# Kernel tuning notes

Hardware: AMD Instinct MI355X
Metric: run time of the kernel (lower is better)

The kernel has to match this reference:

```python
import jax, jax.numpy as jnp
from jax import lax
import numpy as np

B, R, NOBJ, SIZE = 16, 64, 32, 64  # batch, rels/image, objs/image, map size


def setup_inputs() -> dict:
    key = jax.random.key(0)
    ks = jax.random.split(key, 8)
    # boxes as (x1, y1, x2, y2) in an arbitrary image coordinate frame
    xy1 = jax.random.uniform(ks[0], (B, NOBJ, 2), dtype=jnp.float32) * 80.0
    wh = jax.random.uniform(ks[1], (B, NOBJ, 2), dtype=jnp.float32) * 40.0 + 2.0
    bboxes = jnp.concatenate([xy1, xy1 + wh], axis=-1)  # [B, NOBJ, 4]
    num_obj = jnp.full((B,), NOBJ, dtype=jnp.int32)
    num_relation = jnp.full((B,), R, dtype=jnp.int32)  # constant -> static tot_num_rels
    object_pairs = jax.random.randint(ks[2], (B, R, 2), 0, NOBJ)
    conv1_w = jax.random.normal(ks[3], (64, 2, 5, 5), dtype=jnp.float32) * 0.1
    conv1_b = jnp.zeros((64,), dtype=jnp.float32)
    conv2_w = jax.random.normal(ks[4], (32, 64, 5, 5), dtype=jnp.float32) * 0.05
    conv2_b = jnp.zeros((32,), dtype=jnp.float32)
    fc_w = jax.random.normal(ks[5], (512, 32), dtype=jnp.float32) * 0.1
    fc_b = jnp.zeros((512,), dtype=jnp.float32)
    return dict(bboxes=bboxes, num_obj=num_obj, num_relation=num_relation,
                object_pairs=object_pairs, conv1_w=conv1_w, conv1_b=conv1_b,
                conv2_w=conv2_w, conv2_b=conv2_b, fc_w=fc_w, fc_b=fc_b)


def _sp_maps(bboxes, object_pairs):
    # Vectorized replacement of the per-relation python loop + get_sp:
    # both boxes of a pair are rescaled into the 64x64 frame of their union
    # box and rasterized as binary masks (iCAN-style 2-channel spatial config).
    Bc, Rc, _ = object_pairs.shape
    pairs = object_pairs.reshape(-1, 2)                      # [T, 2]
    b_idx = jnp.repeat(jnp.arange(Bc), Rc)                   # [T]
    b0 = bboxes[b_idx, pairs[:, 0]]                          # [T, 4]
    b1 = bboxes[b_idx, pairs[:, 1]]                          # [T, 4]
    ux1 = jnp.minimum(b0[:, 0], b1[:, 0])
    uy1 = jnp.minimum(b0[:, 1], b1[:, 1])
    ux2 = jnp.maximum(b0[:, 2], b1[:, 2])
    uy2 = jnp.maximum(b0[:, 3], b1[:, 3])
    uw = jnp.maximum(ux2 - ux1, 1e-6)
    uh = jnp.maximum(uy2 - uy1, 1e-6)

    def scale(b):  # union-normalized box in [0, SIZE] grid coords
        return jnp.stack([(b[:, 0] - ux1) / uw * SIZE,
                          (b[:, 1] - uy1) / uh * SIZE,
                          (b[:, 2] - ux1) / uw * SIZE,
                          (b[:, 3] - uy1) / uh * SIZE], axis=-1)

    coords = jnp.arange(SIZE, dtype=jnp.float32) + 0.5
    gx = coords[None, None, :]   # [1, 1, SIZE]
    gy = coords[None, :, None]   # [1, SIZE, 1]

    def rasterize(sb):  # sb: [T, 4] -> [T, SIZE, SIZE]
        x1 = sb[:, 0, None, None]; y1 = sb[:, 1, None, None]
        x2 = sb[:, 2, None, None]; y2 = sb[:, 3, None, None]
        return ((gx >= x1) & (gx <= x2) & (gy >= y1) & (gy <= y2)).astype(jnp.float32)

    return jnp.stack([rasterize(scale(b0)), rasterize(scale(b1))], axis=1)  # [T,2,64,64]


def _conv(x, w, b):
    y = lax.conv_general_dilated(x, w, window_strides=(1, 1), padding='VALID',
                                 dimension_numbers=('NCHW', 'OIHW', 'NCHW'))
    return y + b[None, :, None, None]


def _maxpool2(x):
    return lax.reduce_window(x, -jnp.inf, lax.max, (1, 1, 2, 2), (1, 1, 2, 2), 'VALID')


def reference(bboxes, num_obj, num_relation, object_pairs,
              conv1_w, conv1_b, conv2_w, conv2_b, fc_w, fc_b):
    sp = _sp_maps(bboxes, object_pairs)        # [T, 2, 64, 64]
    x = _maxpool2(_conv(sp, conv1_w, conv1_b)) # [T, 64, 30, 30]
    x = _maxpool2(_conv(x, conv2_w, conv2_b))  # [T, 32, 13, 13]
    x = jnp.mean(x, axis=(2, 3))               # AvgPool((13,13)) -> [T, 32]
    return jax.nn.relu(x @ fc_w.T + fc_b)      # [T, 512]
```

## Files before the change

### kernel.cpp

```cpp
#include <hip/hip_runtime.h>
#include <stdint.h>

typedef unsigned long long u64;
typedef short v8s __attribute__((ext_vector_type(8)));
typedef float v4f __attribute__((ext_vector_type(4)));

__device__ __forceinline__ unsigned short f2bf_rne(float f) {
  union { float f; unsigned u; } c; c.f = f;
  unsigned u = c.u;
  u += 0x7fffu + ((u >> 16) & 1u);
  return (unsigned short)(u >> 16);
}

__device__ __forceinline__ void bacc(uint4 z, uint4 a, float* S) {
  const unsigned* zp = &z.x;
  const unsigned* ap = &a.x;
  #pragma unroll
  for (int k = 0; k < 4; k++) {
    unsigned zu = zp[k], au = ap[k];
    S[2 * k]     += __uint_as_float(zu << 16)         - __uint_as_float(au << 16);
    S[2 * k + 1] += __uint_as_float(zu & 0xffff0000u) - __uint_as_float(au & 0xffff0000u);
  }
}


__global__ __launch_bounds__(512) void prepack_g(
    const float* __restrict__ w1,
    unsigned short* __restrict__ Gt)
{
  int e = blockIdx.x * 512 + threadIdx.x;
  int ch = e / 6144, r = e - ch * 6144;
  int cls = r / 384, r2 = r - cls * 384;
  int j = r2 / 64, cout = r2 - j * 64;
  float v = 0.f;
  if (cls > 0) {
    int ia = 0, ib = 0;
    #pragma unroll
    for (int bb = 0; bb < 5; bb++) {
      int base = (bb * (bb + 1)) / 2 + 1;
      if (cls >= base && cls <= base + bb) { ib = bb; ia = cls - base; }
    }
    for (int i = ia; i <= ib; i++)
      for (int jj = 0; jj < j; jj++)
        v += w1[(cout * 2 + ch) * 25 + i * 5 + jj];
  }
  Gt[e] = f2bf_rne(v);
}

__global__ __launch_bounds__(512, 8) void conv1_kernel(
    const float* __restrict__ bboxes,
    const int*   __restrict__ pairs,
    const unsigned short* __restrict__ Gt,
    const float* __restrict__ b1,
    const float* __restrict__ w2,
    unsigned short* __restrict__ XsG,
    unsigned short* __restrict__ Wr)
{
  const int t = threadIdx.x;
  if (blockIdx.x >= 1024) {
    int bb2 = blockIdx.x - 1024;
    #pragma unroll
    for (int r = 0; r < 4; r++) {
      int idx = bb2 * 2048 + r * 512 + t;
      int c = idx / 1600, rem = idx - c * 1600;
      int h = rem / 800, r2 = rem - h * 800;
      int tap = r2 >> 5, chh = r2 & 31;
      Wr[h * 25600 + c * 800 + r2] =
          f2bf_rne(w2[(c * 64 + h * 32 + chh) * 25 + tap]);
    }
    return;
  }
  extern __shared__ char smem[];

  const int n = blockIdx.x;
  const int lane = t & 63;

  {
    const uint4* src = (const uint4*)Gt;
    uint4* dst = (uint4*)smem;
    #pragma unroll
    for (int i = 0; i < 3; i++) dst[t + i * 512] = src[t + i * 512];
  }

  const int bb = n >> 6, rr_ = n & 63;
  const int p0 = pairs[(bb * 64 + rr_) * 2 + 0];
  const int p1 = pairs[(bb * 64 + rr_) * 2 + 1];
  const float* A  = bboxes + (bb * 32 + p0) * 4;
  const float* Bq = bboxes + (bb * 32 + p1) * 4;
  const float ax1 = A[0],  ay1 = A[1],  ax2 = A[2],  ay2 = A[3];
  const float cx1 = Bq[0], cy1 = Bq[1], cx2 = Bq[2], cy2 = Bq[3];
  const float ux1 = fminf(ax1, cx1), uy1 = fminf(ay1, cy1);
  const float ux2 = fmaxf(ax2, cx2), uy2 = fmaxf(ay2, cy2);
  const float uw = fmaxf(ux2 - ux1, 1e-6f), uh = fmaxf(uy2 - uy1, 1e-6f);
  const float g = (float)lane + 0.5f;
  u64 ixs[2], iys[2];
  {
    float X1 = (ax1 - ux1) / uw * 64.f, X2 = (ax2 - ux1) / uw * 64.f;
    float Y1 = (ay1 - uy1) / uh * 64.f, Y2 = (ay2 - uy1) / uh * 64.f;
    ixs[0] = __ballot(g >= X1 && g <= X2);
    iys[0] = __ballot(g >= Y1 && g <= Y2);
  }
  {
    float X1 = (cx1 - ux1) / uw * 64.f, X2 = (cx2 - ux1) / uw * 64.f;
    float Y1 = (cy1 - uy1) / uh * 64.f, Y2 = (cy2 - uy1) / uh * 64.f;
    ixs[1] = __ballot(g >= X1 && g <= X2);
    iys[1] = __ballot(g >= Y1 && g <= Y2);
  }
  __syncthreads();

  const int cg = t & 7, cgo = cg * 16, pr = t >> 3;
  const int hW = cg >> 2;
  float b1v[8];
  #pragma unroll
  for (int i = 0; i < 8; i++) b1v[i] = b1[cg * 8 + i];
  char* const Xbase = (char*)XsG + (u64)n * 115200 + hW * 57600;
  for (int pass = 0; pass < 15; pass++) {
    int pix = pr + (pass << 6);
    if (pix < 900) {
      int qy = pix / 30, qx = pix - qy * 30;
      int cb[2][2], ja_[2][2], jb_[2][2];
      #pragma unroll
      for (int ch = 0; ch < 2; ch++) {
        #pragma unroll
        for (int dy = 0; dy < 2; dy++) {
          unsigned m = (unsigned)(iys[ch] >> (2 * qy + dy)) & 31u;
          int ia = __ffs((int)m) - 1; if (ia < 0) ia = 0;
          int ib = 31 - __clz((int)(m | 1u));
          int cls = m ? (((ib * (ib + 1)) >> 1) + ia + 1) : 0;
          cb[ch][dy] = (ch * 16 + cls) * 768 + cgo;
        }
        #pragma unroll
        for (int dx = 0; dx < 2; dx++) {
          unsigned mx = (unsigned)(ixs[ch] >> (2 * qx + dx)) & 31u;
          int ja = __ffs((int)mx) - 1; if (ja < 0) ja = 0;
          int jbp = mx ? (32 - __clz((int)mx)) : 0;
          ja_[ch][dx] = ja * 128; jb_[ch][dx] = jbp * 128;
        }
      }
      float V[8];
      #pragma unroll
      for (int dy = 0; dy < 2; dy++) {
        #pragma unroll
        for (int dx = 0; dx < 2; dx++) {
          float S[8] = {0, 0, 0, 0, 0, 0, 0, 0};
          #pragma unroll
          for (int ch = 0; ch < 2; ch++) {
            uint4 z = *(const uint4*)(smem + cb[ch][dy] + jb_[ch][dx]);
            uint4 a = *(const uint4*)(smem + cb[ch][dy] + ja_[ch][dx]);
            bacc(z, a, S);
          }
          #pragma unroll
          for (int k = 0; k < 8; k++)
            V[k] = (dy == 0 && dx == 0) ? S[k] : fmaxf(V[k], S[k]);
        }
      }
      uint4 pk;
      unsigned* pkp = &pk.x;
      #pragma unroll
      for (int k = 0; k < 4; k++) {
        unsigned lo = (unsigned)f2bf_rne(V[2 * k]     + b1v[2 * k]);
        unsigned hi = (unsigned)f2bf_rne(V[2 * k + 1] + b1v[2 * k + 1]);
        pkp[k] = lo | (hi << 16);
      }
      int slot = ((cg & 3) + pix) & 3;
      *(uint4*)(Xbase + pix * 64 + slot * 16) = pk;
    }
  }
}

__global__ __launch_bounds__(512, 4) void conv2_kernel(
    const unsigned short* __restrict__ XsG,
    const unsigned short* __restrict__ Wr,
    const float* __restrict__ b2,
    const float* __restrict__ fcw,
    const float* __restrict__ fcb,
    float* __restrict__ out)
{
  extern __shared__ char smem[];
  float* partial = (float*)(smem + 57600);
  float* fs      = (float*)(smem + 58432);
  float* Cout    = (float*)smem;

  const int n = blockIdx.x, t = threadIdx.x;
  const int lane = t & 63, wv = t >> 6;
  const int q = lane >> 4, ln = lane & 15;

  v4f acc[6][2];
  int pclamp[6], psB[6];
  int cnt = 0;
  #pragma unroll
  for (int it = 0; it < 6; it++) {
    int nt = wv + it * 8;
    if (nt < 43) {
      int p = nt * 16 + ln; if (p > 675) p = 675;
      pclamp[it] = p;
      int y = p / 26, x = p - y * 26;
      psB[it] = y * 30 + x;
      cnt = it + 1;
    } else { pclamp[it] = 0; psB[it] = 0; }
    acc[it][0] = (v4f)0.f; acc[it][1] = (v4f)0.f;
  }

  const char* Xg = (const char*)XsG + (u64)n * 115200;
  for (int h = 0; h < 2; h++) {
    if (h) __syncthreads();
    {
      const char* src = Xg + h * 57600;
      #pragma unroll
      for (int k = 0; k < 7; k++) {
        int ci = k * 512 + t;
        __builtin_amdgcn_global_load_lds(
            (const __attribute__((address_space(1))) unsigned int*)(src + ci * 16),
            (__attribute__((address_space(3))) unsigned int*)(smem + ci * 16),
            16, 0, 0);
      }
      if (t < 16) {
        int ci = 3584 + t;
        __builtin_amdgcn_global_load_lds(
            (const __attribute__((address_space(1))) unsigned int*)(src + ci * 16),
            (__attribute__((address_space(3))) unsigned int*)(smem + ci * 16),
            16, 0, 0);
      }
    }
    __syncthreads();

    const unsigned short* pA0 = Wr + h * 25600 + ln * 800 + q * 8;
    const unsigned short* pA1 = pA0 + 16 * 800;
    for (int i = 0; i < 5; i++) {
      #pragma unroll
      for (int j = 0; j < 5; j++) {
        const int tap = i * 5 + j;
        v8s a0 = *(const v8s*)(pA0 + tap * 32);
        v8s a1 = *(const v8s*)(pA1 + tap * 32);
        #pragma unroll
        for (int it = 0; it < 6; it++) {
          if (it < cnt) {
            int ps = psB[it] + i * 30 + j;
            int addr = (ps << 6) + (((q + ps) & 3) << 4);
            v8s b = *(const v8s*)(smem + addr);
            acc[it][0] = __builtin_amdgcn_mfma_f32_16x16x32_bf16(a0, b, acc[it][0], 0, 0, 0);
            acc[it][1] = __builtin_amdgcn_mfma_f32_16x16x32_bf16(a1, b, acc[it][1], 0, 0, 0);
          }
        }
      }
    }
  }

  #pragma unroll
  for (int mt = 0; mt < 2; mt++) {
    __syncthreads();
    #pragma unroll
    for (int it = 0; it < 6; it++) {
      if (it < cnt) {
        #pragma unroll
        for (int r = 0; r < 4; r++)
          Cout[(q * 4 + r) * 677 + pclamp[it]] = acc[it][mt][r];
      }
    }
    __syncthreads();
    if (t < 208) {
      int c = t & 15, py = t >> 4;
      const float* r0 = Cout + c * 677 + (2 * py) * 26;
      const float* r1 = r0 + 26;
      float s = 0.f;
      #pragma unroll
      for (int px = 0; px < 13; px++) {
        float m0 = fmaxf(r0[2 * px], r0[2 * px + 1]);
        float m1 = fmaxf(r1[2 * px], r1[2 * px + 1]);
        s += fmaxf(m0, m1);
      }
      partial[t] = s;
    }
    __syncthreads();
    if (t < 16) {
      float s = 0.f;
      #pragma unroll
      for (int k = 0; k < 13; k++) s += partial[k * 16 + t];
      fs[mt * 16 + t] = s * (1.f / 169.f) + b2[mt * 16 + t];
    }
  }
  __syncthreads();

  {
    const float* wrow = fcw + t * 32;
    float d = 0.f;
    #pragma unroll
    for (int k = 0; k < 32; k++) d += wrow[k] * fs[k];
    out[(u64)n * 512 + t] = fmaxf(d + fcb[t], 0.f);
  }
}


__global__ __launch_bounds__(256) void prepack(
    const float* __restrict__ w1, const float* __restrict__ w2,
    unsigned short* __restrict__ Wr, unsigned short* __restrict__ Gt) {
  int idx = blockIdx.x * 256 + threadIdx.x;
  if (idx < 51200) {
    int c = idx / 1600, rem = idx - c * 1600;
    int ch = rem & 63, tap = rem >> 6;
    Wr[idx] = f2bf_rne(w2[(c * 64 + ch) * 25 + tap]);
  } else if (idx < 51200 + 12288) {
    int e = idx - 51200;
    int ch = e / 6144, r = e - ch * 6144;
    int cls = r / 384, r2 = r - cls * 384;
    int j = r2 / 64, cout = r2 - j * 64;
    float v = 0.f;
    if (cls > 0) {
      int ia = 0, ib = 0;
      for (int bb = 0; bb < 5; bb++) {
        int base = (bb * (bb + 1)) / 2 + 1;
        if (cls >= base && cls <= base + bb) { ib = bb; ia = cls - base; }
      }
      for (int i = ia; i <= ib; i++)
        for (int jj = 0; jj < j; jj++)
          v += w1[(cout * 2 + ch) * 25 + i * 5 + jj];
    }
    Gt[e] = f2bf_rne(v);
  }
}

__global__ __launch_bounds__(512, 2) void fused_kernel(
    const float* __restrict__ bboxes, const int* __restrict__ pairs,
    const unsigned short* __restrict__ Gt, const float* __restrict__ b1,
    const unsigned short* __restrict__ Wr, const float* __restrict__ b2,
    const float* __restrict__ fcw, const float* __restrict__ fcb,
    float* __restrict__ out)
{
  extern __shared__ char smem[];
  float* partial = (float*)(smem + 146976);
  float* fs      = (float*)(smem + 147808);
  float* Cout    = (float*)smem;

  const int n = blockIdx.x, t = threadIdx.x;
  const int lane = t & 63, wv = t >> 6;
  const int q = lane >> 4, ln = lane & 15;

  {
    const uint4* src = (const uint4*)Gt;
    uint4* dst = (uint4*)(smem + 122400);
    #pragma unroll
    for (int i = 0; i < 3; i++) dst[t + i * 512] = src[t + i * 512];
  }
  const int bb = n >> 6, rr_ = n & 63;
  const int p0 = pairs[(bb * 64 + rr_) * 2 + 0];
  const int p1 = pairs[(bb * 64 + rr_) * 2 + 1];
  const float* A  = bboxes + (bb * 32 + p0) * 4;
  const float* Bq = bboxes + (bb * 32 + p1) * 4;
  const float ax1 = A[0],  ay1 = A[1],  ax2 = A[2],  ay2 = A[3];
  const float cx1 = Bq[0], cy1 = Bq[1], cx2 = Bq[2], cy2 = Bq[3];
  const float ux1 = fminf(ax1, cx1), uy1 = fminf(ay1, cy1);
  const float ux2 = fmaxf(ax2, cx2), uy2 = fmaxf(ay2, cy2);
  const float uw = fmaxf(ux2 - ux1, 1e-6f), uh = fmaxf(uy2 - uy1, 1e-6f);
  const float g = (float)lane + 0.5f;
  u64 ixs[2], iys[2];
  {
    float X1 = (ax1 - ux1) / uw * 64.f, X2 = (ax2 - ux1) / uw * 64.f;
    float Y1 = (ay1 - uy1) / uh * 64.f, Y2 = (ay2 - uy1) / uh * 64.f;
    ixs[0] = __ballot(g >= X1 && g <= X2);
    iys[0] = __ballot(g >= Y1 && g <= Y2);
  }
  {
    float X1 = (cx1 - ux1) / uw * 64.f, X2 = (cx2 - ux1) / uw * 64.f;
    float Y1 = (cy1 - uy1) / uh * 64.f, Y2 = (cy2 - uy1) / uh * 64.f;
    ixs[1] = __ballot(g >= X1 && g <= X2);
    iys[1] = __ballot(g >= Y1 && g <= Y2);
  }
  __syncthreads();

  {
    const int cg = t & 7, cgo = cg * 16, pr = t >> 3;
    float b1v[8];
    #pragma unroll
    for (int i = 0; i < 8; i++) b1v[i] = b1[cg * 8 + i];
    for (int pass = 0; pass < 15; pass++) {
      int pix = pr + (pass << 6);
      if (pix < 900) {
        int qy = pix / 30, qx = pix - qy * 30;
        int cb[2][2], ja_[2][2], jb_[2][2];
        #pragma unroll
        for (int ch = 0; ch < 2; ch++) {
          #pragma unroll
          for (int dy = 0; dy < 2; dy++) {
            unsigned m = (unsigned)(iys[ch] >> (2 * qy + dy)) & 31u;
            int ia = __ffs((int)m) - 1; if (ia < 0) ia = 0;
            int ib = 31 - __clz((int)(m | 1u));
            int cls = m ? (((ib * (ib + 1)) >> 1) + ia + 1) : 0;
            cb[ch][dy] = 122400 + (ch * 16 + cls) * 768 + cgo;
          }
          #pragma unroll
          for (int dx = 0; dx < 2; dx++) {
            unsigned mx = (unsigned)(ixs[ch] >> (2 * qx + dx)) & 31u;
            int ja = __ffs((int)mx) - 1; if (ja < 0) ja = 0;
            int jbp = mx ? (32 - __clz((int)mx)) : 0;
            ja_[ch][dx] = ja * 128; jb_[ch][dx] = jbp * 128;
          }
        }
        float V[8];
        #pragma unroll
        for (int dy = 0; dy < 2; dy++) {
          #pragma unroll
          for (int dx = 0; dx < 2; dx++) {
            float S[8] = {0, 0, 0, 0, 0, 0, 0, 0};
            #pragma unroll
            for (int ch = 0; ch < 2; ch++) {
              uint4 z = *(const uint4*)(smem + cb[ch][dy] + jb_[ch][dx]);
              uint4 a = *(const uint4*)(smem + cb[ch][dy] + ja_[ch][dx]);
              bacc(z, a, S);
            }
            #pragma unroll
            for (int k = 0; k < 8; k++)
              V[k] = (dy == 0 && dx == 0) ? S[k] : fmaxf(V[k], S[k]);
          }
        }
        unsigned dws[4];
        #pragma unroll
        for (int k = 0; k < 4; k++) {
          unsigned lo = (unsigned)f2bf_rne(V[2 * k]     + b1v[2 * k]);
          unsigned hi = (unsigned)f2bf_rne(V[2 * k + 1] + b1v[2 * k + 1]);
          dws[k] = lo | (hi << 16);
        }
        uint2 s0; s0.x = dws[0]; s0.y = dws[1];
        uint2 s1; s1.x = dws[2]; s1.y = dws[3];
        *(uint2*)(smem + pix * 136 + cgo) = s0;
        *(uint2*)(smem + pix * 136 + cgo + 8) = s1;
      }
    }
  }
  __syncthreads();

  v4f acc[6][2];
  int pclamp[6], baseB[6];
  int cnt = 0;
  #pragma unroll
  for (int it = 0; it < 6; it++) {
    int nt = wv + it * 8;
    if (nt < 43) {
      int p = nt * 16 + ln; if (p > 675) p = 675;
      pclamp[it] = p;
      int y = p / 26, x = p - y * 26;
      baseB[it] = (y * 30 + x) * 136 + q * 16;
      cnt = it + 1;
    } else { pclamp[it] = 0; baseB[it] = 0; }
    acc[it][0] = (v4f)0.f; acc[it][1] = (v4f)0.f;
  }
  const unsigned short* pA0 = Wr + ln * 1600 + q * 8;
  const unsigned short* pA1 = pA0 + 16 * 1600;
  for (int i5 = 0; i5 < 5; i5++) {
    const int ro = i5 * 4080;
    #pragma unroll
    for (int jt = 0; jt < 5; jt++) {
      #pragma unroll
      for (int hh = 0; hh < 2; hh++) {
        const int s = (i5 * 5 + jt) * 2 + hh;
        v8s a0 = *(const v8s*)(pA0 + s * 32);
        v8s a1 = *(const v8s*)(pA1 + s * 32);
        const int off = ro + jt * 136 + hh * 64;
        #pragma unroll
        for (int it = 0; it < 6; it++) {
          if (it < cnt) {
            uint2 lo = *(const uint2*)(smem + (baseB[it] + off));
            uint2 hi = *(const uint2*)(smem + (baseB[it] + off + 8));
            uint4 bv; bv.x = lo.x; bv.y = lo.y; bv.z = hi.x; bv.w = hi.y;
            v8s b = __builtin_bit_cast(v8s, bv);
            acc[it][0] = __builtin_amdgcn_mfma_f32_16x16x32_bf16(a0, b, acc[it][0], 0, 0, 0);
            acc[it][1] = __builtin_amdgcn_mfma_f32_16x16x32_bf16(a1, b, acc[it][1], 0, 0, 0);
          }
        }
      }
    }
  }
  #pragma unroll
  for (int mt = 0; mt < 2; mt++) {
    __syncthreads();
    #pragma unroll
    for (int it = 0; it < 6; it++) {
      if (it < cnt) {
        #pragma unroll
        for (int r = 0; r < 4; r++)
          Cout[(q * 4 + r) * 677 + pclamp[it]] = acc[it][mt][r];
      }
    }
    __syncthreads();
    if (t < 208) {
      int c = t & 15, py = t >> 4;
      const float* r0 = Cout + c * 677 + (2 * py) * 26;
      const float* r1 = r0 + 26;
      float s = 0.f;
      #pragma unroll
      for (int px = 0; px < 13; px++) {
        float m0 = fmaxf(r0[2 * px], r0[2 * px + 1]);
        float m1 = fmaxf(r1[2 * px], r1[2 * px + 1]);
        s += fmaxf(m0, m1);
      }
      partial[t] = s;
    }
    __syncthreads();
    if (t < 16) {
      float s = 0.f;
      #pragma unroll
      for (int k = 0; k < 13; k++) s += partial[k * 16 + t];
      fs[mt * 16 + t] = s * (1.f / 169.f) + b2[mt * 16 + t];
    }
  }
  __syncthreads();
  {
    const float* wrow = fcw + t * 32;
    float d = 0.f;
    #pragma unroll
    for (int k = 0; k < 32; k++) d += wrow[k] * fs[k];
    out[(u64)n * 512 + t] = fmaxf(d + fcb[t], 0.f);
  }
}

extern "C" void kernel_launch(void* const* d_in, const int* in_sizes, int n_in,
                              void* d_out, int out_size, void* d_ws, size_t ws_size,
                              hipStream_t stream) {
  const float* bboxes = (const float*)d_in[0];
  const int*   pairs  = (const int*)  d_in[3];
  const float* w1     = (const float*)d_in[4];
  const float* b1     = (const float*)d_in[5];
  const float* w2     = (const float*)d_in[6];
  const float* b2     = (const float*)d_in[7];
  const float* fcw    = (const float*)d_in[8];
  const float* fcb    = (const float*)d_in[9];
  float* out = (float*)d_out;

  const u64 xs_bytes = (u64)1024 * 115200;
  if (ws_size >= xs_bytes + 102400) {
    unsigned short* XsG = (unsigned short*)d_ws;
    unsigned short* Wr  = (unsigned short*)((char*)d_ws + xs_bytes);
    unsigned short* Gt  = (unsigned short*)d_out;
    prepack_g<<<24, 512, 0, stream>>>(w1, Gt);
    conv1_kernel<<<1049, 512, 24576, stream>>>(bboxes, pairs, Gt, b1, w2, XsG, Wr);
    conv2_kernel<<<1024, 512, 58560, stream>>>(XsG, Wr, b2, fcw, fcb, out);
  } else {
    unsigned short* Wr = (unsigned short*)d_ws;
    unsigned short* Gt = (unsigned short*)((char*)d_ws + 102400);
    prepack<<<248, 256, 0, stream>>>(w1, w2, Wr, Gt);
    fused_kernel<<<1024, 512, 147936, stream>>>(bboxes, pairs, Gt, b1, Wr, b2,
                                                fcw, fcb, out);
  }
}
```

Baseline: 232.2 us.

## Fuse conv1 rasterization into conv2 kernel, dropping global intermediate buffer

The separate conv1 kernel wrote a large bf16 pooled-activation tensor to the workspace, which conv2 then read back. Now each conv2 block recomputes its pair's conv1 output for one 32-channel half at a time directly into LDS, using a prepacked half-split lookup table. Conv2 MFMA work then consumes that LDS tile. The intermediate is about 118 MB of global writes and reads, and this removes that traffic plus one launch. In exchange, the conv1 work no longer overlaps with conv2 across kernels, and LDS per block grows, which may limit occupancy.

Result: slower. 332.0 us (+43.0%).

```diff
diff --git a/kernel.cpp b/kernel.cpp
--- a/kernel.cpp
+++ b/kernel.cpp
@@ -24,152 +24,48 @@
 }
 
 
-__global__ __launch_bounds__(512) void prepack_g(
+__global__ __launch_bounds__(512) void prepack2(
     const float* __restrict__ w1,
-    unsigned short* __restrict__ Gt)
+    const float* __restrict__ w2,
+    unsigned short* __restrict__ Wr,
+    unsigned short* __restrict__ Gt2)
 {
-  int e = blockIdx.x * 512 + threadIdx.x;
-  int ch = e / 6144, r = e - ch * 6144;
-  int cls = r / 384, r2 = r - cls * 384;
-  int j = r2 / 64, cout = r2 - j * 64;
-  float v = 0.f;
-  if (cls > 0) {
-    int ia = 0, ib = 0;
-    #pragma unroll
-    for (int bb = 0; bb < 5; bb++) {
-      int base = (bb * (bb + 1)) / 2 + 1;
-      if (cls >= base && cls <= base + bb) { ib = bb; ia = cls - base; }
-    }
-    for (int i = ia; i <= ib; i++)
-      for (int jj = 0; jj < j; jj++)
-        v += w1[(cout * 2 + ch) * 25 + i * 5 + jj];
-  }
-  Gt[e] = f2bf_rne(v);
-}
-
-__global__ __launch_bounds__(512, 8) void conv1_kernel(
+  int idx = blockIdx.x * 512 + threadIdx.x;
+  if (idx < 51200) {
+    int c = idx / 1600, rem = idx - c * 1600;
+    int h = rem / 800, r2 = rem - h * 800;
+    int tap = r2 >> 5, chh = r2 & 31;
+    Wr[h * 25600 + c * 800 + r2] =
+        f2bf_rne(w2[(c * 64 + h * 32 + chh) * 25 + tap]);
+  } else {
+    int e = idx - 51200;
+    int c32 = e & 31;
+    int j   = (e >> 5) % 6;
+    int cls = (e / 192) & 15;
+    int ch  = (e / 3072) & 1;
+    int h   = e / 6144;
+    int cout = h * 32 + c32;
+    float v = 0.f;
+    if (cls > 0) {
+      int ia = 0, ib = 0;
+      #pragma unroll
+      for (int bb = 0; bb < 5; bb++) {
+        int base = (bb * (bb + 1)) / 2 + 1;
+        if (cls >= base && cls <= base + bb) { ib = bb; ia = cls - base; }
+      }
+      for (int i = ia; i <= ib; i++)
+        for (int jj = 0; jj < j; jj++)
+          v += w1[(cout * 2 + ch) * 25 + i * 5 + jj];
+    }
+    Gt2[e] = f2bf_rne(v);
+  }
+}
+
+__global__ __launch_bounds__(512, 4) void conv2f_kernel(
     const float* __restrict__ bboxes,
     const int*   __restrict__ pairs,
-    const unsigned short* __restrict__ Gt,
+    const unsigned short* __restrict__ Gt2,
     const float* __restrict__ b1,
-    const float* __restrict__ w2,
-    unsigned short* __restrict__ XsG,
-    unsigned short* __restrict__ Wr)
-{
-  const int t = threadIdx.x;
-  if (blockIdx.x >= 1024) {
-    int bb2 = blockIdx.x - 1024;
-    #pragma unroll
-    for (int r = 0; r < 4; r++) {
-      int idx = bb2 * 2048 + r * 512 + t;
-      int c = idx / 1600, rem = idx - c * 1600;
-      int h = rem / 800, r2 = rem - h * 800;
-      int tap = r2 >> 5, chh = r2 & 31;
-      Wr[h * 25600 + c * 800 + r2] =
-          f2bf_rne(w2[(c * 64 + h * 32 + chh) * 25 + tap]);
-    }
-    return;
-  }
-  extern __shared__ char smem[];
-
-  const int n = blockIdx.x;
-  const int lane = t & 63;
-
-  {
-    const uint4* src = (const uint4*)Gt;
-    uint4* dst = (uint4*)smem;
-    #pragma unroll
-    for (int i = 0; i < 3; i++) dst[t + i * 512] = src[t + i * 512];
-  }
-
-  const int bb = n >> 6, rr_ = n & 63;
-  const int p0 = pairs[(bb * 64 + rr_) * 2 + 0];
-  const int p1 = pairs[(bb * 64 + rr_) * 2 + 1];
-  const float* A  = bboxes + (bb * 32 + p0) * 4;
-  const float* Bq = bboxes + (bb * 32 + p1) * 4;
-  const float ax1 = A[0],  ay1 = A[1],  ax2 = A[2],  ay2 = A[3];
-  const float cx1 = Bq[0], cy1 = Bq[1], cx2 = Bq[2], cy2 = Bq[3];
-  const float ux1 = fminf(ax1, cx1), uy1 = fminf(ay1, cy1);
-  const float ux2 = fmaxf(ax2, cx2), uy2 = fmaxf(ay2, cy2);
-  const float uw = fmaxf(ux2 - ux1, 1e-6f), uh = fmaxf(uy2 - uy1, 1e-6f);
-  const float g = (float)lane + 0.5f;
-  u64 ixs[2], iys[2];
-  {
-    float X1 = (ax1 - ux1) / uw * 64.f, X2 = (ax2 - ux1) / uw * 64.f;
-    float Y1 = (ay1 - uy1) / uh * 64.f, Y2 = (ay2 - uy1) / uh * 64.f;
-    ixs[0] = __ballot(g >= X1 && g <= X2);
-    iys[0] = __ballot(g >= Y1 && g <= Y2);
-  }
-  {
-    float X1 = (cx1 - ux1) / uw * 64.f, X2 = (cx2 - ux1) / uw * 64.f;
-    float Y1 = (cy1 - uy1) / uh * 64.f, Y2 = (cy2 - uy1) / uh * 64.f;
-    ixs[1] = __ballot(g >= X1 && g <= X2);
-    iys[1] = __ballot(g >= Y1 && g <= Y2);
-  }
-  __syncthreads();
-
-  const int cg = t & 7, cgo = cg * 16, pr = t >> 3;
-  const int hW = cg >> 2;
-  float b1v[8];
-  #pragma unroll
-  for (int i = 0; i < 8; i++) b1v[i] = b1[cg * 8 + i];
-  char* const Xbase = (char*)XsG + (u64)n * 115200 + hW * 57600;
-  for (int pass = 0; pass < 15; pass++) {
-    int pix = pr + (pass << 6);
-    if (pix < 900) {
-      int qy = pix / 30, qx = pix - qy * 30;
-      int cb[2][2], ja_[2][2], jb_[2][2];
-      #pragma unroll
-      for (int ch = 0; ch < 2; ch++) {
-        #pragma unroll
-        for (int dy = 0; dy < 2; dy++) {
-          unsigned m = (unsigned)(iys[ch] >> (2 * qy + dy)) & 31u;
-          int ia = __ffs((int)m) - 1; if (ia < 0) ia = 0;
-          int ib = 31 - __clz((int)(m | 1u));
-          int cls = m ? (((ib * (ib + 1)) >> 1) + ia + 1) : 0;
-          cb[ch][dy] = (ch * 16 + cls) * 768 + cgo;
-        }
-        #pragma unroll
-        for (int dx = 0; dx < 2; dx++) {
-          unsigned mx = (unsigned)(ixs[ch] >> (2 * qx + dx)) & 31u;
-          int ja = __ffs((int)mx) - 1; if (ja < 0) ja = 0;
-          int jbp = mx ? (32 - __clz((int)mx)) : 0;
-          ja_[ch][dx] = ja * 128; jb_[ch][dx] = jbp * 128;
-        }
-      }
-      float V[8];
-      #pragma unroll
-      for (int dy = 0; dy < 2; dy++) {
-        #pragma unroll
-        for (int dx = 0; dx < 2; dx++) {
-          float S[8] = {0, 0, 0, 0, 0, 0, 0, 0};
-          #pragma unroll
-          for (int ch = 0; ch < 2; ch++) {
-            uint4 z = *(const uint4*)(smem + cb[ch][dy] + jb_[ch][dx]);
-            uint4 a = *(const uint4*)(smem + cb[ch][dy] + ja_[ch][dx]);
-            bacc(z, a, S);
-          }
-          #pragma unroll
-          for (int k = 0; k < 8; k++)
-            V[k] = (dy == 0 && dx == 0) ? S[k] : fmaxf(V[k], S[k]);
-        }
-      }
-      uint4 pk;
-      unsigned* pkp = &pk.x;
-      #pragma unroll
-      for (int k = 0; k < 4; k++) {
-        unsigned lo = (unsigned)f2bf_rne(V[2 * k]     + b1v[2 * k]);
-        unsigned hi = (unsigned)f2bf_rne(V[2 * k + 1] + b1v[2 * k + 1]);
-        pkp[k] = lo | (hi << 16);
-      }
-      int slot = ((cg & 3) + pix) & 3;
-      *(uint4*)(Xbase + pix * 64 + slot * 16) = pk;
-    }
-  }
-}
-
-__global__ __launch_bounds__(512, 4) void conv2_kernel(
-    const unsigned short* __restrict__ XsG,
     const unsigned short* __restrict__ Wr,
     const float* __restrict__ b2,
     const float* __restrict__ fcw,
@@ -184,45 +80,123 @@
   const int n = blockIdx.x, t = threadIdx.x;
   const int lane = t & 63, wv = t >> 6;
   const int q = lane >> 4, ln = lane & 15;
+  const int cnt = (wv < 3) ? 6 : 5;
 
   v4f acc[6][2];
-  int pclamp[6], psB[6];
-  int cnt = 0;
   #pragma unroll
-  for (int it = 0; it < 6; it++) {
-    int nt = wv + it * 8;
-    if (nt < 43) {
-      int p = nt * 16 + ln; if (p > 675) p = 675;
-      pclamp[it] = p;
-      int y = p / 26, x = p - y * 26;
-      psB[it] = y * 30 + x;
-      cnt = it + 1;
-    } else { pclamp[it] = 0; psB[it] = 0; }
-    acc[it][0] = (v4f)0.f; acc[it][1] = (v4f)0.f;
-  }
-
-  const char* Xg = (const char*)XsG + (u64)n * 115200;
+  for (int it = 0; it < 6; it++) { acc[it][0] = (v4f)0.f; acc[it][1] = (v4f)0.f; }
+
   for (int h = 0; h < 2; h++) {
     if (h) __syncthreads();
     {
-      const char* src = Xg + h * 57600;
-      #pragma unroll
-      for (int k = 0; k < 7; k++) {
-        int ci = k * 512 + t;
+      const char* gsrc = (const char*)Gt2 + h * 12288;
+      __builtin_amdgcn_global_load_lds(
+          (const __attribute__((address_space(1))) unsigned int*)(gsrc + t * 16),
+          (__attribute__((address_space(3))) unsigned int*)(smem + 57600 + t * 16),
+          16, 0, 0);
+      if (t < 256) {
         __builtin_amdgcn_global_load_lds(
-            (const __attribute__((address_space(1))) unsigned int*)(src + ci * 16),
-            (__attribute__((address_space(3))) unsigned int*)(smem + ci * 16),
+            (const __attribute__((address_space(1))) unsigned int*)(gsrc + (512 + t) * 16),
+            (__attribute__((address_space(3))) unsigned int*)(smem + 57600 + (512 + t) * 16),
             16, 0, 0);
       }
-      if (t < 16) {
-        int ci = 3584 + t;
-        __builtin_amdgcn_global_load_lds(
-            (const __attribute__((address_space(1))) unsigned int*)(src + ci * 16),
-            (__attribute__((address_space(3))) unsigned int*)(smem + ci * 16),
-            16, 0, 0);
-      }
-    }
-    __syncthreads();
+    }
+    u64 ixs[2], iys[2];
+    {
+      const int bb = n >> 6, rr_ = n & 63;
+      const int p0 = pairs[(bb * 64 + rr_) * 2 + 0];
+      const int p1 = pairs[(bb * 64 + rr_) * 2 + 1];
+      const float* A  = bboxes + (bb * 32 + p0) * 4;
+      const float* Bq = bboxes + (bb * 32 + p1) * 4;
+      const float ax1 = A[0],  ay1 = A[1],  ax2 = A[2],  ay2 = A[3];
+      const float cx1 = Bq[0], cy1 = Bq[1], cx2 = Bq[2], cy2 = Bq[3];
+      const float ux1 = fminf(ax1, cx1), uy1 = fminf(ay1, cy1);
+      const float ux2 = fmaxf(ax2, cx2), uy2 = fmaxf(ay2, cy2);
+      const float uw = fmaxf(ux2 - ux1, 1e-6f), uh = fmaxf(uy2 - uy1, 1e-6f);
+      const float g = (float)lane + 0.5f;
+      {
+        float X1 = (ax1 - ux1) / uw * 64.f, X2 = (ax2 - ux1) / uw * 64.f;
+        float Y1 = (ay1 - uy1) / uh * 64.f, Y2 = (ay2 - uy1) / uh * 64.f;
+        ixs[0] = __ballot(g >= X1 && g <= X2);
+        iys[0] = __ballot(g >= Y1 && g <= Y2);
+      }
+      {
+        float X1 = (cx1 - ux1) / uw * 64.f, X2 = (cx2 - ux1) / uw * 64.f;
+        float Y1 = (cy1 - uy1) / uh * 64.f, Y2 = (cy2 - uy1) / uh * 64.f;
+        ixs[1] = __ballot(g >= X1 && g <= X2);
+        iys[1] = __ballot(g >= Y1 && g <= Y2);
+      }
+    }
+    __syncthreads();
+
+    {
+      const int cg4 = t & 3, cgo = cg4 * 16, pr4 = t >> 2;
+      float b1v[8];
+      #pragma unroll
+      for (int i = 0; i < 8; i++) b1v[i] = b1[h * 32 + cg4 * 8 + i];
+      for (int pass = 0; pass < 8; pass++) {
+        int pix = pr4 + (pass << 7);
+        if (pix < 900) {
+          int qy = pix / 30, qx = pix - qy * 30;
+          int cb[2][2], ja_[2][2], jb_[2][2];
+          #pragma unroll
+          for (int ch = 0; ch < 2; ch++) {
+            #pragma unroll
+            for (int dy = 0; dy < 2; dy++) {
+              unsigned m = (unsigned)(iys[ch] >> (2 * qy + dy)) & 31u;
+              int ia = __ffs((int)m) - 1; if (ia < 0) ia = 0;
+              int ib = 31 - __clz((int)(m | 1u));
+              int cls = m ? (((ib * (ib + 1)) >> 1) + ia + 1) : 0;
+              cb[ch][dy] = 57600 + (ch * 16 + cls) * 384 + cgo;
+            }
+            #pragma unroll
+            for (int dx = 0; dx < 2; dx++) {
+              unsigned mx = (unsigned)(ixs[ch] >> (2 * qx + dx)) & 31u;
+              int ja = __ffs((int)mx) - 1; if (ja < 0) ja = 0;
+              int jbp = mx ? (32 - __clz((int)mx)) : 0;
+              ja_[ch][dx] = ja * 64; jb_[ch][dx] = jbp * 64;
+            }
+          }
+          float V[8];
+          #pragma unroll
+          for (int dy = 0; dy < 2; dy++) {
+            #pragma unroll
+            for (int dx = 0; dx < 2; dx++) {
+              float S[8] = {0, 0, 0, 0, 0, 0, 0, 0};
+              #pragma unroll
+              for (int ch = 0; ch < 2; ch++) {
+                uint4 z = *(const uint4*)(smem + cb[ch][dy] + jb_[ch][dx]);
+                uint4 a = *(const uint4*)(smem + cb[ch][dy] + ja_[ch][dx]);
+                bacc(z, a, S);
+              }
+              #pragma unroll
+              for (int k = 0; k < 8; k++)
+                V[k] = (dy == 0 && dx == 0) ? S[k] : fmaxf(V[k], S[k]);
+            }
+          }
+          uint4 pk;
+          unsigned* pkp = &pk.x;
+          #pragma unroll
+          for (int k = 0; k < 4; k++) {
+            unsigned lo = (unsigned)f2bf_rne(V[2 * k]     + b1v[2 * k]);
+            unsigned hi = (unsigned)f2bf_rne(V[2 * k + 1] + b1v[2 * k + 1]);
+            pkp[k] = lo | (hi << 16);
+          }
+          int slot = (cg4 + pix) & 3;
+          *(uint4*)(smem + pix * 64 + slot * 16) = pk;
+        }
+      }
+    }
+    __syncthreads();
+
+    int psB[6];
+    #pragma unroll
+    for (int it = 0; it < 6; it++) {
+      int nt = wv + it * 8;
+      int p = nt * 16 + ln; if (p > 675) p = 675;
+      int y = p / 26, x = p - y * 26;
+      psB[it] = (nt < 43) ? (y * 30 + x) : 0;
+    }
 
     const unsigned short* pA0 = Wr + h * 25600 + ln * 800 + q * 8;
     const unsigned short* pA1 = pA0 + 16 * 800;
@@ -252,9 +226,10 @@
     #pragma unroll
     for (int it = 0; it < 6; it++) {
       if (it < cnt) {
+        int p = (wv + it * 8) * 16 + ln; if (p > 675) p = 675;
         #pragma unroll
         for (int r = 0; r < 4; r++)
-          Cout[(q * 4 + r) * 677 + pclamp[it]] = acc[it][mt][r];
+          Cout[(q * 4 + r) * 677 + p] = acc[it][mt][r];
       }
     }
     __syncthreads();
@@ -525,14 +500,12 @@
   const float* fcb    = (const float*)d_in[9];
   float* out = (float*)d_out;
 
-  const u64 xs_bytes = (u64)1024 * 115200;
-  if (ws_size >= xs_bytes + 102400) {
-    unsigned short* XsG = (unsigned short*)d_ws;
-    unsigned short* Wr  = (unsigned short*)((char*)d_ws + xs_bytes);
-    unsigned short* Gt  = (unsigned short*)d_out;
-    prepack_g<<<24, 512, 0, stream>>>(w1, Gt);
-    conv1_kernel<<<1049, 512, 24576, stream>>>(bboxes, pairs, Gt, b1, w2, XsG, Wr);
-    conv2_kernel<<<1024, 512, 58560, stream>>>(XsG, Wr, b2, fcw, fcb, out);
+  if (ws_size >= 126976) {
+    unsigned short* Wr  = (unsigned short*)d_ws;
+    unsigned short* Gt2 = (unsigned short*)((char*)d_ws + 102400);
+    prepack2<<<124, 512, 0, stream>>>(w1, w2, Wr, Gt2);
+    conv2f_kernel<<<1024, 512, 69888, stream>>>(bboxes, pairs, Gt2, b1, Wr, b2,
+                                                fcw, fcb, out);
   } else {
     unsigned short* Wr = (unsigned short*)d_ws;
     unsigned short* Gt = (unsigned short*)((char*)d_ws + 102400);
```
